# Kernel optimization log

Hardware: AMD Instinct MI355X
Metric: run time of the kernel (lower is better)

The kernel has to match this reference:

```python
import jax, jax.numpy as jnp
import numpy as np

TOP_K = 2

def _moe_forward(x, gate_w, w1, w2, w3):
    # x: [B,S,H] -> tokens [T,H]
    B, S, H = x.shape
    xt = x.reshape(-1, H)                              # [T,H]
    T = xt.shape[0]
    E = gate_w.shape[0]
    # router
    logits = xt @ gate_w.T                             # [T,E]
    probs = jax.nn.softmax(logits.astype(jnp.float32), axis=-1)
    rw, sel = jax.lax.top_k(probs, TOP_K)              # [T,K]
    rw = rw / jnp.sum(rw, axis=-1, keepdims=True)
    # per-token per-expert combine weight (0 if expert not selected)
    combine = jnp.zeros((T, E), dtype=xt.dtype).at[
        jnp.arange(T)[:, None], sel].add(rw.astype(xt.dtype))  # [T,E]
    # dense per-expert SwiGLU FFN over all tokens (prefill path of module)
    h1 = jnp.einsum('th,efh->tef', xt, w1)             # [T,E,F]
    h3 = jnp.einsum('th,efh->tef', xt, w3)             # [T,E,F]
    g = jax.nn.silu(h1) * h3                           # [T,E,F]
    g = g * combine[:, :, None]                        # apply routing weight before down-proj
    out = jnp.einsum('tef,ehf->th', g, w2)             # [T,H]
    return out.reshape(B, S, H)


def setup_inputs() -> dict:
    key = jax.random.key(0)
    ks = jax.random.split(key, 5)
    B, S, H, F, E = 2, 2048, 1024, 3584, 8
    scale = 1.0 / np.sqrt(H)
    return {
        'hidden_states': jax.random.normal(ks[0], (B, S, H), jnp.float32),
        'gate_w': jax.random.normal(ks[1], (E, H), jnp.float32) * scale,
        'w1': jax.random.normal(ks[2], (E, F, H), jnp.float32) * scale,
        'w2': jax.random.normal(ks[3], (E, H, F), jnp.float32) * (1.0 / np.sqrt(F)),
        'w3': jax.random.normal(ks[4], (E, F, H), jnp.float32) * scale,
    }


def reference(hidden_states, gate_w, w1, w2, w3):
    return _moe_forward(hidden_states, gate_w, w1, w2, w3)
```

## Files before the change

kernel.cpp:

```cpp
#include <hip/hip_runtime.h>
#include <hip/hip_bf16.h>

#define TT   4096
#define HH   1024
#define FF   3584
#define EE   8
#define N13  7168
#define TKP  8192

#define BM 128
#define BN 128
#define BK 64

typedef unsigned short u16;
typedef __attribute__((ext_vector_type(8))) short short8;
typedef __attribute__((ext_vector_type(4))) float floatx4;

__device__ __forceinline__ u16 f2b(float f) {
  union { float f; unsigned u; } v; v.f = f;
  unsigned r = v.u + 0x7FFFu + ((v.u >> 16) & 1u);
  return (u16)(r >> 16);
}

__device__ __forceinline__ void gld_lds16(const u16* g, u16* l) {
  __builtin_amdgcn_global_load_lds((const __attribute__((address_space(1))) unsigned int*)g,
                                   (__attribute__((address_space(3))) unsigned int*)l,
                                   16, 0, 0);
}

__global__ __launch_bounds__(256) void cvt_x(const float4* __restrict__ in, ushort4* __restrict__ outp) {
  int i = blockIdx.x * 256 + threadIdx.x;
  float4 v = in[i];
  ushort4 o; o.x = f2b(v.x); o.y = f2b(v.y); o.z = f2b(v.z); o.w = f2b(v.w);
  outp[i] = o;
}

__global__ __launch_bounds__(256) void cvt_w13(const float* __restrict__ w1, const float* __restrict__ w3,
                                               ushort4* __restrict__ w13i) {
  int i = blockIdx.x * 256 + threadIdx.x;
  const int perE = N13 * (HH / 4);
  int e = i / perE;
  int rem = i - e * perE;
  int n = rem / (HH / 4);
  int h4 = rem - n * (HH / 4);
  int f = ((n >> 5) << 4) + (n & 15);
  int sel = (n >> 4) & 1;
  const float* base = sel ? w3 : w1;
  const float4* src = ((const float4*)(base + (size_t)(e * FF + f) * HH)) + h4;
  float4 v = *src;
  ushort4 o; o.x = f2b(v.x); o.y = f2b(v.y); o.z = f2b(v.z); o.w = f2b(v.w);
  w13i[i] = o;
}

__global__ __launch_bounds__(256) void cvt_w2(const float4* __restrict__ in, ushort4* __restrict__ outp) {
  int i = blockIdx.x * 256 + threadIdx.x;
  float4 v = in[i];
  ushort4 o; o.x = f2b(v.x); o.y = f2b(v.y); o.z = f2b(v.z); o.w = f2b(v.w);
  outp[i] = o;
}

__global__ __launch_bounds__(256) void router(const float* __restrict__ x, const float* __restrict__ gw,
                                              int* __restrict__ cnt, int* __restrict__ tok_list,
                                              float* __restrict__ wt_list) {
  int lane = threadIdx.x & 63;
  int wv = threadIdx.x >> 6;
  int t = blockIdx.x * 4 + wv;
  const float* xp = x + (size_t)t * HH;
  float acc[EE];
#pragma unroll
  for (int e = 0; e < EE; e++) acc[e] = 0.f;
  for (int h = lane; h < HH; h += 64) {
    float xv = xp[h];
#pragma unroll
    for (int e = 0; e < EE; e++) acc[e] += xv * gw[e * HH + h];
  }
#pragma unroll
  for (int e = 0; e < EE; e++) {
#pragma unroll
    for (int off = 32; off > 0; off >>= 1) acc[e] += __shfl_xor(acc[e], off, 64);
  }
  if (lane == 0) {
    int i1 = 0;
#pragma unroll
    for (int e = 1; e < EE; e++) if (acc[e] > acc[i1]) i1 = e;
    int i2 = -1;
#pragma unroll
    for (int e = 0; e < EE; e++) {
      if (e == i1) continue;
      if (i2 < 0 || acc[e] > acc[i2]) i2 = e;
    }
    float wA = 1.f / (1.f + __expf(acc[i2] - acc[i1]));
    float wB = 1.f - wA;
    int p1 = atomicAdd(cnt + i1, 1);
    tok_list[i1 * TT + p1] = t; wt_list[i1 * TT + p1] = wA;
    int p2 = atomicAdd(cnt + i2, 1);
    tok_list[i2 * TT + p2] = t; wt_list[i2 * TT + p2] = wB;
  }
}

__global__ void mk_offsets(const int* __restrict__ cnt, int* __restrict__ offs) {
  if (threadIdx.x == 0) {
    int s = 0;
    for (int e = 0; e < EE; e++) { offs[e] = s; s += cnt[e]; }
  }
}

__global__ __launch_bounds__(256) void pairmap(const int* __restrict__ cnt, const int* __restrict__ offs,
                                               const int* __restrict__ tok_list,
                                               int* __restrict__ tokp) {
  int i = blockIdx.x * 256 + threadIdx.x;
  int e = i >> 12;
  int s = i & (TT - 1);
  if (s < cnt[e]) {
    tokp[offs[e] + s] = tok_list[i];
  }
}

__global__ __launch_bounds__(256) void gemm_a(const u16* __restrict__ xb, const u16* __restrict__ w13i,
                                              const int* __restrict__ cnt, const int* __restrict__ offs,
                                              const int* __restrict__ tok_list, const float* __restrict__ wt_list,
                                              u16* __restrict__ gbuf) {
  const int ntile = blockIdx.x;
  const int e = blockIdx.y >> 5;
  const int rt = blockIdx.y & 31;
  const int cn = cnt[e];
  if (rt * BM >= cn) return;

  __shared__ u16 As[BM * BK];
  __shared__ u16 Bs[BN * BK];
  __shared__ int toks[BM];
  __shared__ float wts[BM];

  const int tid = threadIdx.x;
  if (tid < BM) {
    int r = rt * BM + tid;
    if (r >= cn) r = cn - 1;
    toks[tid] = tok_list[e * TT + r];
    wts[tid] = wt_list[e * TT + r];
  }
  __syncthreads();

  const u16* aptr[4];
  const u16* bptr[4];
  u16* alds[4];
  u16* blds[4];
#pragma unroll
  for (int i = 0; i < 4; i++) {
    int row = (tid >> 3) + i * 32;
    int c8 = (tid & 7) ^ (row & 7);
    aptr[i] = xb + (size_t)toks[row] * HH + c8 * 8;
    bptr[i] = w13i + ((size_t)e * N13 + (size_t)ntile * BN + row) * HH + c8 * 8;
    alds[i] = As + row * BK + (tid & 7) * 8;
    blds[i] = Bs + row * BK + (tid & 7) * 8;
  }

  const int lane = tid & 63;
  const int wv = tid >> 6;
  const int wr = (wv >> 1) * 64;
  const int wc = (wv & 1) * 64;
  const int fr = lane & 15;
  const int fk8 = lane >> 4;

  floatx4 acc[4][4];
#pragma unroll
  for (int mi = 0; mi < 4; mi++)
#pragma unroll
    for (int ni = 0; ni < 4; ni++)
#pragma unroll
      for (int q = 0; q < 4; q++) acc[mi][ni][q] = 0.f;

  for (int k0 = 0; k0 < HH; k0 += BK) {
#pragma unroll
    for (int i = 0; i < 4; i++) {
      gld_lds16(aptr[i], alds[i]); aptr[i] += BK;
      gld_lds16(bptr[i], blds[i]); bptr[i] += BK;
    }
    __syncthreads();
#pragma unroll
    for (int ks = 0; ks < 2; ks++) {
      int c8 = (ks * 4 + fk8) ^ (fr & 7);
      short8 af[4], bfr[4];
#pragma unroll
      for (int mi = 0; mi < 4; mi++) af[mi] = *(const short8*)&As[(wr + mi * 16 + fr) * BK + c8 * 8];
#pragma unroll
      for (int ni = 0; ni < 4; ni++) bfr[ni] = *(const short8*)&Bs[(wc + ni * 16 + fr) * BK + c8 * 8];
#pragma unroll
      for (int mi = 0; mi < 4; mi++)
#pragma unroll
        for (int ni = 0; ni < 4; ni++)
          acc[mi][ni] = __builtin_amdgcn_mfma_f32_16x16x32_bf16(af[mi], bfr[ni], acc[mi][ni], 0, 0, 0);
    }
    __syncthreads();
  }

  const int gofs = offs[e];
  const int cl = lane & 15;
#pragma unroll
  for (int mi = 0; mi < 4; mi++) {
#pragma unroll
    for (int q = 0; q < 4; q++) {
      int r = wr + mi * 16 + (lane >> 4) * 4 + q;
      int gr = rt * BM + r;
      if (gr < cn) {
        float w = wts[r];
        u16* dst = gbuf + (size_t)(gofs + gr) * FF + (size_t)ntile * 64 + wc / 2 + cl;
#pragma unroll
        for (int pg = 0; pg < 2; pg++) {
          float h1 = acc[mi][2 * pg][q];
          float h3 = acc[mi][2 * pg + 1][q];
          float s = h1 / (1.f + __expf(-h1));
          dst[pg * 16] = f2b(s * h3 * w);
        }
      }
    }
  }
}

__global__ __launch_bounds__(256) void gemm_b(const u16* __restrict__ g, const u16* __restrict__ w2b,
                                              const int* __restrict__ cnt, const int* __restrict__ offs,
                                              const int* __restrict__ tokp, float* __restrict__ out) {
  const int ntile = blockIdx.x;
  const int e = blockIdx.y >> 5;
  const int rt = blockIdx.y & 31;
  const int cn = cnt[e];
  if (rt * BM >= cn) return;
  const int gofs = offs[e];

  __shared__ u16 As[BM * BK];
  __shared__ u16 Bs[BN * BK];
  __shared__ int toks[BM];

  const int tid = threadIdx.x;
  if (tid < BM) {
    int r = rt * BM + tid;
    if (r >= cn) r = cn - 1;
    toks[tid] = tokp[gofs + r];
  }
  __syncthreads();

  const u16* aptr[4];
  const u16* bptr[4];
  u16* alds[4];
  u16* blds[4];
#pragma unroll
  for (int i = 0; i < 4; i++) {
    int row = (tid >> 3) + i * 32;
    int gr = rt * BM + row;
    if (gr >= cn) gr = cn - 1;
    int c8 = (tid & 7) ^ (row & 7);
    aptr[i] = g + (size_t)(gofs + gr) * FF + c8 * 8;
    bptr[i] = w2b + ((size_t)e * HH + (size_t)ntile * BN + row) * FF + c8 * 8;
    alds[i] = As + row * BK + (tid & 7) * 8;
    blds[i] = Bs + row * BK + (tid & 7) * 8;
  }

  const int lane = tid & 63;
  const int wv = tid >> 6;
  const int wr = (wv >> 1) * 64;
  const int wc = (wv & 1) * 64;
  const int fr = lane & 15;
  const int fk8 = lane >> 4;

  floatx4 acc[4][4];
#pragma unroll
  for (int mi = 0; mi < 4; mi++)
#pragma unroll
    for (int ni = 0; ni < 4; ni++)
#pragma unroll
      for (int q = 0; q < 4; q++) acc[mi][ni][q] = 0.f;

  for (int k0 = 0; k0 < FF; k0 += BK) {
#pragma unroll
    for (int i = 0; i < 4; i++) {
      gld_lds16(aptr[i], alds[i]); aptr[i] += BK;
      gld_lds16(bptr[i], blds[i]); bptr[i] += BK;
    }
    __syncthreads();
#pragma unroll
    for (int ks = 0; ks < 2; ks++) {
      int c8 = (ks * 4 + fk8) ^ (fr & 7);
      short8 af[4], bfr[4];
#pragma unroll
      for (int mi = 0; mi < 4; mi++) af[mi] = *(const short8*)&As[(wr + mi * 16 + fr) * BK + c8 * 8];
#pragma unroll
      for (int ni = 0; ni < 4; ni++) bfr[ni] = *(const short8*)&Bs[(wc + ni * 16 + fr) * BK + c8 * 8];
#pragma unroll
      for (int mi = 0; mi < 4; mi++)
#pragma unroll
        for (int ni = 0; ni < 4; ni++)
          acc[mi][ni] = __builtin_amdgcn_mfma_f32_16x16x32_bf16(af[mi], bfr[ni], acc[mi][ni], 0, 0, 0);
    }
    __syncthreads();
  }

#pragma unroll
  for (int mi = 0; mi < 4; mi++) {
#pragma unroll
    for (int q = 0; q < 4; q++) {
      int r = wr + mi * 16 + (lane >> 4) * 4 + q;
      int gr = rt * BM + r;
      if (gr < cn) {
        int tk = toks[r];
        float* dst = out + (size_t)tk * HH + (size_t)ntile * BN + wc + (lane & 15);
#pragma unroll
        for (int ni = 0; ni < 4; ni++) atomicAdd(dst + ni * 16, acc[mi][ni][q]);
      }
    }
  }
}

extern "C" void kernel_launch(void* const* d_in, const int* in_sizes, int n_in,
                              void* d_out, int out_size, void* d_ws, size_t ws_size,
                              hipStream_t stream) {
  const float* x  = (const float*)d_in[0];
  const float* gw = (const float*)d_in[1];
  const float* w1 = (const float*)d_in[2];
  const float* w2 = (const float*)d_in[3];
  const float* w3 = (const float*)d_in[4];
  float* out = (float*)d_out;

  char* ws = (char*)d_ws;
  u16* xb    = (u16*)ws;  ws += (size_t)TT * HH * 2;
  u16* w13i  = (u16*)ws;  ws += (size_t)EE * N13 * HH * 2;
  u16* w2b   = (u16*)ws;  ws += (size_t)EE * HH * FF * 2;
  u16* gbuf  = (u16*)ws;  ws += (size_t)TKP * FF * 2;
  int* cnt   = (int*)ws;  ws += 256;
  int* offs  = (int*)ws;  ws += 256;
  int* tok_list = (int*)ws;   ws += (size_t)EE * TT * 4;
  float* wt_list = (float*)ws; ws += (size_t)EE * TT * 4;
  int* tokp  = (int*)ws;  ws += (size_t)TKP * 4;

  hipMemsetAsync(cnt, 0, 256, stream);
  hipMemsetAsync(out, 0, (size_t)TT * HH * 4, stream);

  cvt_x<<<(TT * HH / 4) / 256, 256, 0, stream>>>((const float4*)x, (ushort4*)xb);
  cvt_w13<<<(EE * N13 * (HH / 4)) / 256, 256, 0, stream>>>(w1, w3, (ushort4*)w13i);
  cvt_w2<<<(EE * HH * (FF / 4)) / 256, 256, 0, stream>>>((const float4*)w2, (ushort4*)w2b);

  router<<<TT / 4, 256, 0, stream>>>(x, gw, cnt, tok_list, wt_list);
  mk_offsets<<<1, 64, 0, stream>>>(cnt, offs);
  pairmap<<<(EE * TT) / 256, 256, 0, stream>>>(cnt, offs, tok_list, tokp);

  gemm_a<<<dim3(N13 / BN, EE * (TT / BM)), 256, 0, stream>>>(xb, w13i, cnt, offs, tok_list, wt_list, gbuf);
  gemm_b<<<dim3(HH / BN, EE * (TT / BM)), 256, 0, stream>>>(gbuf, w2b, cnt, offs, tokp, out);
}
```

Baseline: 738.2 us.

## Fuse prep kernels, drop offsets kernel, split-K down-proj, reorder grid

Merges the weight/activation conversions and the router into a single prep launch, and removes the offsets kernel by computing prefix sums inline from the counts. The down-projection GEMM is split four ways along K to add parallelism, relying on atomic accumulation into the zeroed output. The grid axes are swapped so consecutive blocks share weight tiles, and the SiLU division uses a reciprocal. Split-K adds extra atomic traffic on the output.

Result: slower. 1.360 ms (+84.2%).

```diff
diff --git a/kernel.cpp b/kernel.cpp
--- a/kernel.cpp
+++ b/kernel.cpp
@@ -11,6 +11,13 @@
 #define BM 128
 #define BN 128
 #define BK 64
+#define KSPLIT 4
+#define KCH (FF / KSPLIT)
+
+#define NB13 57344
+#define NBW2 28672
+#define NBX  4096
+#define NBR  1024
 
 typedef unsigned short u16;
 typedef __attribute__((ext_vector_type(8))) short short8;
@@ -28,102 +35,116 @@
                                    16, 0, 0);
 }
 
-__global__ __launch_bounds__(256) void cvt_x(const float4* __restrict__ in, ushort4* __restrict__ outp) {
-  int i = blockIdx.x * 256 + threadIdx.x;
-  float4 v = in[i];
-  ushort4 o; o.x = f2b(v.x); o.y = f2b(v.y); o.z = f2b(v.z); o.w = f2b(v.w);
-  outp[i] = o;
-}
-
-__global__ __launch_bounds__(256) void cvt_w13(const float* __restrict__ w1, const float* __restrict__ w3,
-                                               ushort4* __restrict__ w13i) {
-  int i = blockIdx.x * 256 + threadIdx.x;
-  const int perE = N13 * (HH / 4);
-  int e = i / perE;
-  int rem = i - e * perE;
-  int n = rem / (HH / 4);
-  int h4 = rem - n * (HH / 4);
-  int f = ((n >> 5) << 4) + (n & 15);
-  int sel = (n >> 4) & 1;
-  const float* base = sel ? w3 : w1;
-  const float4* src = ((const float4*)(base + (size_t)(e * FF + f) * HH)) + h4;
-  float4 v = *src;
-  ushort4 o; o.x = f2b(v.x); o.y = f2b(v.y); o.z = f2b(v.z); o.w = f2b(v.w);
-  w13i[i] = o;
-}
-
-__global__ __launch_bounds__(256) void cvt_w2(const float4* __restrict__ in, ushort4* __restrict__ outp) {
-  int i = blockIdx.x * 256 + threadIdx.x;
-  float4 v = in[i];
-  ushort4 o; o.x = f2b(v.x); o.y = f2b(v.y); o.z = f2b(v.z); o.w = f2b(v.w);
-  outp[i] = o;
-}
-
-__global__ __launch_bounds__(256) void router(const float* __restrict__ x, const float* __restrict__ gw,
-                                              int* __restrict__ cnt, int* __restrict__ tok_list,
-                                              float* __restrict__ wt_list) {
-  int lane = threadIdx.x & 63;
-  int wv = threadIdx.x >> 6;
-  int t = blockIdx.x * 4 + wv;
-  const float* xp = x + (size_t)t * HH;
-  float acc[EE];
-#pragma unroll
-  for (int e = 0; e < EE; e++) acc[e] = 0.f;
-  for (int h = lane; h < HH; h += 64) {
-    float xv = xp[h];
-#pragma unroll
-    for (int e = 0; e < EE; e++) acc[e] += xv * gw[e * HH + h];
-  }
-#pragma unroll
-  for (int e = 0; e < EE; e++) {
-#pragma unroll
-    for (int off = 32; off > 0; off >>= 1) acc[e] += __shfl_xor(acc[e], off, 64);
-  }
-  if (lane == 0) {
-    int i1 = 0;
-#pragma unroll
-    for (int e = 1; e < EE; e++) if (acc[e] > acc[i1]) i1 = e;
-    int i2 = -1;
+__device__ __forceinline__ void cnt_offs(const int* __restrict__ cnt, int e, int& cn, int& gofs) {
+  int s = 0, c = 0;
+#pragma unroll
+  for (int i = 0; i < EE; i++) {
+    int v = cnt[i];
+    if (i < e) s += v;
+    if (i == e) c = v;
+  }
+  cn = c; gofs = s;
+}
+
+__global__ __launch_bounds__(256) void prep(const float* __restrict__ x, const float* __restrict__ gw,
+                                            const float* __restrict__ w1, const float* __restrict__ w2,
+                                            const float* __restrict__ w3,
+                                            ushort4* __restrict__ w13i, ushort4* __restrict__ w2b,
+                                            ushort4* __restrict__ xb,
+                                            int* __restrict__ cnt, int* __restrict__ tok_list,
+                                            float* __restrict__ wt_list) {
+  int bid = blockIdx.x;
+  if (bid < NB13) {
+    int i = bid * 256 + threadIdx.x;
+    const int perE = N13 * (HH / 4);
+    int e = i / perE;
+    int rem = i - e * perE;
+    int n = rem / (HH / 4);
+    int h4 = rem - n * (HH / 4);
+    int f = ((n >> 5) << 4) + (n & 15);
+    int sel = (n >> 4) & 1;
+    const float* base = sel ? w3 : w1;
+    const float4* src = ((const float4*)(base + (size_t)(e * FF + f) * HH)) + h4;
+    float4 v = *src;
+    ushort4 o; o.x = f2b(v.x); o.y = f2b(v.y); o.z = f2b(v.z); o.w = f2b(v.w);
+    w13i[i] = o;
+    return;
+  }
+  bid -= NB13;
+  if (bid < NBW2) {
+    int i = bid * 256 + threadIdx.x;
+    float4 v = ((const float4*)w2)[i];
+    ushort4 o; o.x = f2b(v.x); o.y = f2b(v.y); o.z = f2b(v.z); o.w = f2b(v.w);
+    w2b[i] = o;
+    return;
+  }
+  bid -= NBW2;
+  if (bid < NBX) {
+    int i = bid * 256 + threadIdx.x;
+    float4 v = ((const float4*)x)[i];
+    ushort4 o; o.x = f2b(v.x); o.y = f2b(v.y); o.z = f2b(v.z); o.w = f2b(v.w);
+    xb[i] = o;
+    return;
+  }
+  bid -= NBX;
+  {
+    int lane = threadIdx.x & 63;
+    int wv = threadIdx.x >> 6;
+    int t = bid * 4 + wv;
+    const float* xp = x + (size_t)t * HH;
+    float acc[EE];
+#pragma unroll
+    for (int e = 0; e < EE; e++) acc[e] = 0.f;
+    for (int h = lane; h < HH; h += 64) {
+      float xv = xp[h];
+#pragma unroll
+      for (int e = 0; e < EE; e++) acc[e] += xv * gw[e * HH + h];
+    }
 #pragma unroll
     for (int e = 0; e < EE; e++) {
-      if (e == i1) continue;
-      if (i2 < 0 || acc[e] > acc[i2]) i2 = e;
-    }
-    float wA = 1.f / (1.f + __expf(acc[i2] - acc[i1]));
-    float wB = 1.f - wA;
-    int p1 = atomicAdd(cnt + i1, 1);
-    tok_list[i1 * TT + p1] = t; wt_list[i1 * TT + p1] = wA;
-    int p2 = atomicAdd(cnt + i2, 1);
-    tok_list[i2 * TT + p2] = t; wt_list[i2 * TT + p2] = wB;
-  }
-}
-
-__global__ void mk_offsets(const int* __restrict__ cnt, int* __restrict__ offs) {
-  if (threadIdx.x == 0) {
-    int s = 0;
-    for (int e = 0; e < EE; e++) { offs[e] = s; s += cnt[e]; }
-  }
-}
-
-__global__ __launch_bounds__(256) void pairmap(const int* __restrict__ cnt, const int* __restrict__ offs,
+#pragma unroll
+      for (int off = 32; off > 0; off >>= 1) acc[e] += __shfl_xor(acc[e], off, 64);
+    }
+    if (lane == 0) {
+      int i1 = 0;
+#pragma unroll
+      for (int e = 1; e < EE; e++) if (acc[e] > acc[i1]) i1 = e;
+      int i2 = -1;
+#pragma unroll
+      for (int e = 0; e < EE; e++) {
+        if (e == i1) continue;
+        if (i2 < 0 || acc[e] > acc[i2]) i2 = e;
+      }
+      float wA = 1.f / (1.f + __expf(acc[i2] - acc[i1]));
+      float wB = 1.f - wA;
+      int p1 = atomicAdd(cnt + i1, 1);
+      tok_list[i1 * TT + p1] = t; wt_list[i1 * TT + p1] = wA;
+      int p2 = atomicAdd(cnt + i2, 1);
+      tok_list[i2 * TT + p2] = t; wt_list[i2 * TT + p2] = wB;
+    }
+  }
+}
+
+__global__ __launch_bounds__(256) void pairmap(const int* __restrict__ cnt,
                                                const int* __restrict__ tok_list,
                                                int* __restrict__ tokp) {
   int i = blockIdx.x * 256 + threadIdx.x;
   int e = i >> 12;
   int s = i & (TT - 1);
-  if (s < cnt[e]) {
-    tokp[offs[e] + s] = tok_list[i];
-  }
+  int cn, gofs;
+  cnt_offs(cnt, e, cn, gofs);
+  if (s < cn) tokp[gofs + s] = tok_list[i];
 }
 
 __global__ __launch_bounds__(256) void gemm_a(const u16* __restrict__ xb, const u16* __restrict__ w13i,
-                                              const int* __restrict__ cnt, const int* __restrict__ offs,
+                                              const int* __restrict__ cnt,
                                               const int* __restrict__ tok_list, const float* __restrict__ wt_list,
                                               u16* __restrict__ gbuf) {
-  const int ntile = blockIdx.x;
-  const int e = blockIdx.y >> 5;
-  const int rt = blockIdx.y & 31;
-  const int cn = cnt[e];
+  const int e = blockIdx.x >> 5;
+  const int rt = blockIdx.x & 31;
+  const int ntile = blockIdx.y;
+  int cn, gofs;
+  cnt_offs(cnt, e, cn, gofs);
   if (rt * BM >= cn) return;
 
   __shared__ u16 As[BM * BK];
@@ -193,7 +214,6 @@
     __syncthreads();
   }
 
-  const int gofs = offs[e];
   const int cl = lane & 15;
 #pragma unroll
   for (int mi = 0; mi < 4; mi++) {
@@ -208,7 +228,7 @@
         for (int pg = 0; pg < 2; pg++) {
           float h1 = acc[mi][2 * pg][q];
           float h3 = acc[mi][2 * pg + 1][q];
-          float s = h1 / (1.f + __expf(-h1));
+          float s = h1 * __builtin_amdgcn_rcpf(1.f + __expf(-h1));
           dst[pg * 16] = f2b(s * h3 * w);
         }
       }
@@ -217,14 +237,15 @@
 }
 
 __global__ __launch_bounds__(256) void gemm_b(const u16* __restrict__ g, const u16* __restrict__ w2b,
-                                              const int* __restrict__ cnt, const int* __restrict__ offs,
+                                              const int* __restrict__ cnt,
                                               const int* __restrict__ tokp, float* __restrict__ out) {
-  const int ntile = blockIdx.x;
-  const int e = blockIdx.y >> 5;
-  const int rt = blockIdx.y & 31;
-  const int cn = cnt[e];
+  const int e = blockIdx.x >> 5;
+  const int rt = blockIdx.x & 31;
+  const int ntile = blockIdx.y;
+  const int ksp = blockIdx.z;
+  int cn, gofs;
+  cnt_offs(cnt, e, cn, gofs);
   if (rt * BM >= cn) return;
-  const int gofs = offs[e];
 
   __shared__ u16 As[BM * BK];
   __shared__ u16 Bs[BN * BK];
@@ -248,8 +269,8 @@
     int gr = rt * BM + row;
     if (gr >= cn) gr = cn - 1;
     int c8 = (tid & 7) ^ (row & 7);
-    aptr[i] = g + (size_t)(gofs + gr) * FF + c8 * 8;
-    bptr[i] = w2b + ((size_t)e * HH + (size_t)ntile * BN + row) * FF + c8 * 8;
+    aptr[i] = g + (size_t)(gofs + gr) * FF + ksp * KCH + c8 * 8;
+    bptr[i] = w2b + ((size_t)e * HH + (size_t)ntile * BN + row) * FF + ksp * KCH + c8 * 8;
     alds[i] = As + row * BK + (tid & 7) * 8;
     blds[i] = Bs + row * BK + (tid & 7) * 8;
   }
@@ -269,7 +290,7 @@
 #pragma unroll
       for (int q = 0; q < 4; q++) acc[mi][ni][q] = 0.f;
 
-  for (int k0 = 0; k0 < FF; k0 += BK) {
+  for (int k0 = 0; k0 < KCH; k0 += BK) {
 #pragma unroll
     for (int i = 0; i < 4; i++) {
       gld_lds16(aptr[i], alds[i]); aptr[i] += BK;
@@ -325,7 +346,6 @@
   u16* w2b   = (u16*)ws;  ws += (size_t)EE * HH * FF * 2;
   u16* gbuf  = (u16*)ws;  ws += (size_t)TKP * FF * 2;
   int* cnt   = (int*)ws;  ws += 256;
-  int* offs  = (int*)ws;  ws += 256;
   int* tok_list = (int*)ws;   ws += (size_t)EE * TT * 4;
   float* wt_list = (float*)ws; ws += (size_t)EE * TT * 4;
   int* tokp  = (int*)ws;  ws += (size_t)TKP * 4;
@@ -333,14 +353,11 @@
   hipMemsetAsync(cnt, 0, 256, stream);
   hipMemsetAsync(out, 0, (size_t)TT * HH * 4, stream);
 
-  cvt_x<<<(TT * HH / 4) / 256, 256, 0, stream>>>((const float4*)x, (ushort4*)xb);
-  cvt_w13<<<(EE * N13 * (HH / 4)) / 256, 256, 0, stream>>>(w1, w3, (ushort4*)w13i);
-  cvt_w2<<<(EE * HH * (FF / 4)) / 256, 256, 0, stream>>>((const float4*)w2, (ushort4*)w2b);
-
-  router<<<TT / 4, 256, 0, stream>>>(x, gw, cnt, tok_list, wt_list);
-  mk_offsets<<<1, 64, 0, stream>>>(cnt, offs);
-  pairmap<<<(EE * TT) / 256, 256, 0, stream>>>(cnt, offs, tok_list, tokp);
-
-  gemm_a<<<dim3(N13 / BN, EE * (TT / BM)), 256, 0, stream>>>(xb, w13i, cnt, offs, tok_list, wt_list, gbuf);
-  gemm_b<<<dim3(HH / BN, EE * (TT / BM)), 256, 0, stream>>>(gbuf, w2b, cnt, offs, tokp, out);
-}
+  prep<<<NB13 + NBW2 + NBX + NBR, 256, 0, stream>>>(x, gw, w1, w2, w3,
+                                                    (ushort4*)w13i, (ushort4*)w2b, (ushort4*)xb,
+                                                    cnt, tok_list, wt_list);
+  pairmap<<<(EE * TT) / 256, 256, 0, stream>>>(cnt, tok_list, tokp);
+
+  gemm_a<<<dim3(EE * 32, N13 / BN), 256, 0, stream>>>(xb, w13i, cnt, tok_list, wt_list, gbuf);
+  gemm_b<<<dim3(EE * 32, HH / BN, KSPLIT), 256, 0, stream>>>(gbuf, w2b, cnt, tokp, out);
+}
```
